# Optimization experiments

Measured on AMD Instinct MI355X. Metric: run time of the kernel, lower is better.

The kernel has to match this reference:

```python
import jax, jax.numpy as jnp
import numpy as np

N_NODES = 50000
N_EDGES = 800000
IN_DIM = 128
HID_DIM = 128
N_CLASSES = 32
X_STEPS = 2
BN_EPS = 1e-5


def _agg(h, src, dst):
    # PyG 'add' aggregation with self-loops: out[i] = sum_{(j->i) in E} h[j] + h[i]
    return jax.ops.segment_sum(h[src], dst, num_segments=h.shape[0]) + h


def setup_inputs() -> dict:
    key = jax.random.key(0)
    ks = jax.random.split(key, 8)
    x = jax.random.normal(ks[0], (N_NODES, IN_DIM), dtype=jnp.float32)
    edge_index = jax.random.randint(ks[1], (2, N_EDGES), 0, N_NODES, dtype=jnp.int64)
    s1 = 1.0 / np.sqrt(IN_DIM)
    W1 = jax.random.uniform(ks[2], (IN_DIM, HID_DIM), jnp.float32, -s1, s1)
    b1 = jax.random.uniform(ks[3], (HID_DIM,), jnp.float32, -s1, s1)
    gamma = jnp.ones((HID_DIM,), jnp.float32)
    beta = jnp.zeros((HID_DIM,), jnp.float32)
    s2 = 1.0 / np.sqrt(HID_DIM)
    W2 = jax.random.uniform(ks[4], (HID_DIM, N_CLASSES), jnp.float32, -s2, s2)
    b2 = jax.random.uniform(ks[5], (N_CLASSES,), jnp.float32, -s2, s2)
    return {"x": x, "edge_index": edge_index, "W1": W1, "b1": b1,
            "gamma": gamma, "beta": beta, "W2": W2, "b2": b2}


def reference(x, edge_index, W1, b1, gamma, beta, W2, b2):
    src, dst = edge_index[0], edge_index[1]
    # conv1: K-step sum aggregation, then Linear
    h = x
    for _ in range(X_STEPS):
        h = _agg(h, src, dst)
    h = h @ W1 + b1
    # BatchNorm (training mode: batch statistics over nodes)
    mu = jnp.mean(h, axis=0)
    var = jnp.mean(jnp.square(h - mu), axis=0)  # biased variance, as torch BN uses
    h = (h - mu) * jax.lax.rsqrt(var + BN_EPS) * gamma + beta
    h = jax.nn.selu(h)
    # dropout p=0.0 -> identity
    # conv2: 1-step aggregation + Linear
    h = _agg(h, src, dst)
    h = h @ W2 + b2
    return jax.nn.softmax(h, axis=1)
```

## Files before the change

### kernel.cpp

```cpp
#include <hip/hip_runtime.h>

#define NN 50000
#define NE 800000
#define DIM 128
#define NC 32
#define CB 782
#define CCH 13
#define EB 8192
#define NBLK 98
#define BN_EPS 1e-5f
#define SELU_ALPHA 1.6732632423543772f
#define SELU_SCALE 1.0507009873554805f

typedef __attribute__((ext_vector_type(8))) short bf16x8;
typedef __attribute__((ext_vector_type(4))) float f32x4;

#define FMA16(acc, hv, w0, w1, w2, w3)                                   \
    acc.x = fmaf(hv.x, w0.x, acc.x); acc.y = fmaf(hv.x, w0.y, acc.y);    \
    acc.z = fmaf(hv.x, w0.z, acc.z); acc.w = fmaf(hv.x, w0.w, acc.w);    \
    acc.x = fmaf(hv.y, w1.x, acc.x); acc.y = fmaf(hv.y, w1.y, acc.y);    \
    acc.z = fmaf(hv.y, w1.z, acc.z); acc.w = fmaf(hv.y, w1.w, acc.w);    \
    acc.x = fmaf(hv.z, w2.x, acc.x); acc.y = fmaf(hv.z, w2.y, acc.y);    \
    acc.z = fmaf(hv.z, w2.z, acc.z); acc.w = fmaf(hv.z, w2.w, acc.w);    \
    acc.x = fmaf(hv.w, w3.x, acc.x); acc.y = fmaf(hv.w, w3.y, acc.y);    \
    acc.z = fmaf(hv.w, w3.z, acc.z); acc.w = fmaf(hv.w, w3.w, acc.w);

#define BNSELU1(v)                                                        \
    v = v > 0.f ? SELU_SCALE * v : SELU_SCALE * SELU_ALPHA * (__expf(v) - 1.f);
#define BNSELU4(hv, sc, sh)                                               \
    hv.x = fmaf(hv.x, sc.x, sh.x); BNSELU1(hv.x)                          \
    hv.y = fmaf(hv.y, sc.y, sh.y); BNSELU1(hv.y)                          \
    hv.z = fmaf(hv.z, sc.z, sh.z); BNSELU1(hv.z)                          \
    hv.w = fmaf(hv.w, sc.w, sh.w); BNSELU1(hv.w)

__device__ __forceinline__ float bf_lo(unsigned u) { return __uint_as_float(u << 16); }
__device__ __forceinline__ float bf_hi(unsigned u) { return __uint_as_float(u & 0xffff0000u); }
__device__ __forceinline__ unsigned bf_round(float a) {
    unsigned ba = __float_as_uint(a);
    return (ba + 0x7fffu + ((ba >> 16) & 1u)) >> 16;
}
__device__ __forceinline__ unsigned pack_bf16(float a, float b) {
    return bf_round(a) | (bf_round(b) << 16);
}

__global__ void k_detect(const int* __restrict__ raw, int* __restrict__ flag,
                         float* __restrict__ z) {
    if (blockIdx.x == 0) {
        if (threadIdx.x < 64) {
            int v = raw[2 * threadIdx.x + 1];
            unsigned long long b = __ballot(v == 0);
            if (threadIdx.x == 0) *flag = (b == 0xFFFFFFFFFFFFFFFFULL) ? 1 : 0;
        }
    } else {
        z[threadIdx.x] = 0.f;
    }
}

#define CVT_BLOCKS 6250
__global__ void k_prep(const float4* __restrict__ in, uint2* __restrict__ out,
                       const float* __restrict__ W1, ushort* __restrict__ w1t) {
    if (blockIdx.x < CVT_BLOCKS) {
        int i = blockIdx.x * 256 + threadIdx.x;
        float4 v = in[i];
        out[i] = make_uint2(pack_bf16(v.x, v.y), pack_bf16(v.z, v.w));
    } else {
        int i = (blockIdx.x - CVT_BLOCKS) * 256 + threadIdx.x;
        if (i < DIM * DIM) {
            int k = i >> 7, n = i & 127;
            w1t[n * 136 + k] = (ushort)bf_round(W1[i]);
        }
    }
}

__global__ __launch_bounds__(256) void k_bcount(const void* __restrict__ raw,
                                                const int* __restrict__ flag,
                                                int* __restrict__ cnt) {
    __shared__ int lh[CB];
    int blk = blockIdx.x, tid = threadIdx.x;
    for (int t = tid; t < CB; t += 256) lh[t] = 0;
    __syncthreads();
    int f = *flag;
    const long long* r64 = (const long long*)raw;
    const int* r32 = (const int*)raw;
    int e0 = blk * EB;
    int n = min(EB, NE - e0);
    for (int i = tid; i < n; i += 256) {
        int d = f ? (int)r64[NE + e0 + i] : r32[NE + e0 + i];
        atomicAdd(&lh[d >> 6], 1);
    }
    __syncthreads();
    for (int t = tid; t < CB; t += 256) cnt[t * NBLK + blk] = lh[t];
}

__global__ void k_colscan(int* __restrict__ cnt, int* __restrict__ tot) {
    int b = blockIdx.x;
    int* row = cnt + b * NBLK;
    int l = threadIdx.x;
    int p0 = 2 * l, p1 = 2 * l + 1;
    int a0 = (p0 < NBLK) ? row[p0] : 0;
    int a1 = (p1 < NBLK) ? row[p1] : 0;
    int s = a0 + a1, inc = s;
    #pragma unroll
    for (int off = 1; off < 64; off <<= 1) {
        int u = __shfl_up(inc, off, 64);
        if (l >= off) inc += u;
    }
    int ex = inc - s;
    if (p0 < NBLK) row[p0] = ex;
    if (p1 < NBLK) row[p1] = ex + a0;
    if (l == 63) tot[b] = inc;
}

__global__ void k_cscan(const int* __restrict__ tot, int* __restrict__ cbase,
                        int* __restrict__ rowptr) {
    int lane = threadIdx.x;
    int base = lane * CCH;
    int loc[CCH];
    int s = 0;
    #pragma unroll
    for (int i = 0; i < CCH; ++i) {
        int idx = base + i;
        int v = (idx < CB) ? tot[idx] : 0;
        loc[i] = s; s += v;
    }
    int inc = s;
    #pragma unroll
    for (int off = 1; off < 64; off <<= 1) {
        int u = __shfl_up(inc, off, 64);
        if (lane >= off) inc += u;
    }
    int ex = inc - s;
    #pragma unroll
    for (int i = 0; i < CCH; ++i) {
        int idx = base + i;
        if (idx < CB) cbase[idx] = ex + loc[i];
    }
    if (lane == 63) { cbase[CB] = inc; rowptr[NN] = NE; }
}

__global__ __launch_bounds__(256) void k_cscatter2(const void* __restrict__ raw,
                                                   const int* __restrict__ flag,
                                                   const int* __restrict__ cnt,
                                                   const int* __restrict__ cbase,
                                                   unsigned* __restrict__ pairs) {
    __shared__ int lh[CB], lbase[CB], lcur[CB], gbase[CB];
    __shared__ unsigned lp[EB];
    int blk = blockIdx.x, tid = threadIdx.x;
    for (int t = tid; t < CB; t += 256) {
        lh[t] = 0;
        gbase[t] = cbase[t] + cnt[t * NBLK + blk];
    }
    __syncthreads();
    int f = *flag;
    const long long* r64 = (const long long*)raw;
    const int* r32 = (const int*)raw;
    int e0 = blk * EB;
    int n = min(EB, NE - e0);
    for (int i = tid; i < n; i += 256) {
        int d = f ? (int)r64[NE + e0 + i] : r32[NE + e0 + i];
        atomicAdd(&lh[d >> 6], 1);
    }
    __syncthreads();
    if (tid < 64) {
        int base = tid * CCH;
        int loc[CCH];
        int s = 0;
        #pragma unroll
        for (int i = 0; i < CCH; ++i) {
            int idx = base + i;
            int v = (idx < CB) ? lh[idx] : 0;
            loc[i] = s; s += v;
        }
        int inc = s;
        #pragma unroll
        for (int off = 1; off < 64; off <<= 1) {
            int u = __shfl_up(inc, off, 64);
            if (tid >= off) inc += u;
        }
        int ex = inc - s;
        #pragma unroll
        for (int i = 0; i < CCH; ++i) {
            int idx = base + i;
            if (idx < CB) lbase[idx] = ex + loc[i];
        }
    }
    __syncthreads();
    for (int t = tid; t < CB; t += 256) lcur[t] = lbase[t];
    __syncthreads();
    for (int i = tid; i < n; i += 256) {
        int d = f ? (int)r64[NE + e0 + i] : r32[NE + e0 + i];
        int sv = f ? (int)r64[e0 + i] : r32[e0 + i];
        int b = d >> 6;
        int p = atomicAdd(&lcur[b], 1);
        lp[p] = (unsigned)sv | ((unsigned)(d & 63) << 16) | ((unsigned)b << 22);
    }
    __syncthreads();
    for (int i = tid; i < n; i += 256) {
        unsigned pr = lp[i];
        int b = pr >> 22;
        pairs[gbase[b] + (i - lbase[b])] = pr;
    }
}

__global__ __launch_bounds__(256) void k_bucket(const unsigned* __restrict__ pairs,
                                                const int* __restrict__ cbase,
                                                int* __restrict__ rowptr,
                                                int* __restrict__ eidx) {
    __shared__ int cnt[64], cur[64];
    int b = blockIdx.x;
    int tid = threadIdx.x;
    if (tid < 64) cnt[tid] = 0;
    __syncthreads();
    int lo = cbase[b], hi = cbase[b + 1];
    for (int i = lo + tid; i < hi; i += 256)
        atomicAdd(&cnt[(pairs[i] >> 16) & 63], 1);
    __syncthreads();
    if (tid < 64) {
        int v = cnt[tid];
        int inc = v;
        #pragma unroll
        for (int off = 1; off < 64; off <<= 1) {
            int u = __shfl_up(inc, off, 64);
            if (tid >= off) inc += u;
        }
        int ex = inc - v;
        cur[tid] = ex;
        int node = b * 64 + tid;
        if (node < NN) rowptr[node] = lo + ex;
    }
    __syncthreads();
    for (int i = lo + tid; i < hi; i += 256) {
        unsigned pr = pairs[i];
        int p = atomicAdd(&cur[(pr >> 16) & 63], 1);
        eidx[lo + p] = (int)(pr & 0xFFFFu);
    }
}

__global__ __launch_bounds__(256) void k_gather_bf(const unsigned* __restrict__ in,
                                                   unsigned* __restrict__ out,
                                                   const int* __restrict__ rowptr,
                                                   const int* __restrict__ eidx) {
    int node = blockIdx.x * 4 + (threadIdx.x >> 6);
    if (node >= NN) return;
    int lane = threadIdx.x & 63;
    unsigned su = in[(size_t)node * 64 + lane];
    float2 acc = {bf_lo(su), bf_hi(su)};
    int b = rowptr[node], e = rowptr[node + 1];
    int j = b;
    for (; j + 3 < e; j += 4) {
        int s0 = eidx[j], s1 = eidx[j + 1], s2 = eidx[j + 2], s3 = eidx[j + 3];
        unsigned u0 = in[(size_t)s0 * 64 + lane];
        unsigned u1 = in[(size_t)s1 * 64 + lane];
        unsigned u2 = in[(size_t)s2 * 64 + lane];
        unsigned u3 = in[(size_t)s3 * 64 + lane];
        acc.x += bf_lo(u0) + bf_lo(u1) + bf_lo(u2) + bf_lo(u3);
        acc.y += bf_hi(u0) + bf_hi(u1) + bf_hi(u2) + bf_hi(u3);
    }
    for (; j < e; ++j) {
        unsigned u0 = in[(size_t)eidx[j] * 64 + lane];
        acc.x += bf_lo(u0);
        acc.y += bf_hi(u0);
    }
    out[(size_t)node * 64 + lane] = pack_bf16(acc.x, acc.y);
}

__global__ __launch_bounds__(256) void k_gemm1(
    const unsigned* __restrict__ hBb, const ushort* __restrict__ w1t,
    const float* __restrict__ b1, float* __restrict__ h1,
    float* __restrict__ ssum, float* __restrict__ ssq) {
    __shared__ __align__(16) ushort wT[DIM * 136];
    __shared__ float redS[4 * DIM];
    __shared__ float redQ[4 * DIM];
    int tid = threadIdx.x;
    for (int i = tid; i < DIM * 136 / 8; i += 256)
        ((uint4*)wT)[i] = ((const uint4*)w1t)[i];
    for (int i = tid; i < 4 * DIM; i += 256) { redS[i] = 0.f; redQ[i] = 0.f; }
    __syncthreads();

    int wid = tid >> 6, lane = tid & 63;
    int cl = lane & 15, kg = lane >> 4;
    int tile = blockIdx.x * 4 + wid;
    if (tile < NN / 16) {
        int rbase = tile * 16;
        const uint4* arow = (const uint4*)(hBb + (size_t)(rbase + cl) * 64);
        f32x4 acc[8];
        #pragma unroll
        for (int ct = 0; ct < 8; ++ct) acc[ct] = (f32x4){0.f, 0.f, 0.f, 0.f};
        #pragma unroll
        for (int kk = 0; kk < 4; ++kk) {
            union { uint4 u; bf16x8 f; } a;
            a.u = arow[kk * 4 + kg];
            #pragma unroll
            for (int ct = 0; ct < 8; ++ct) {
                union { uint4 u; bf16x8 f; } bb;
                bb.u = *(const uint4*)&wT[(ct * 16 + cl) * 136 + kk * 32 + kg * 8];
                acc[ct] = __builtin_amdgcn_mfma_f32_16x16x32_bf16(a.f, bb.f, acc[ct], 0, 0, 0);
            }
        }
        #pragma unroll
        for (int ct = 0; ct < 8; ++ct) {
            int col = ct * 16 + cl;
            float bias = b1[col];
            float s = 0.f, q = 0.f;
            #pragma unroll
            for (int i = 0; i < 4; ++i) {
                float v = acc[ct][i] + bias;
                h1[(size_t)(rbase + kg * 4 + i) * DIM + col] = v;
                s += v; q += v * v;
            }
            s += __shfl_xor(s, 16); s += __shfl_xor(s, 32);
            q += __shfl_xor(q, 16); q += __shfl_xor(q, 32);
            if (kg == 0) { redS[wid * DIM + col] = s; redQ[wid * DIM + col] = q; }
        }
    }
    __syncthreads();
    if (tid < DIM) {
        float S = redS[tid] + redS[DIM + tid] + redS[2 * DIM + tid] + redS[3 * DIM + tid];
        float Q = redQ[tid] + redQ[DIM + tid] + redQ[2 * DIM + tid] + redQ[3 * DIM + tid];
        atomicAdd(&ssum[tid], S);
        atomicAdd(&ssq[tid], Q);
    }
}

__global__ __launch_bounds__(256) void k_gemm2(const float* __restrict__ h,
                                               const float* __restrict__ W2,
                                               const float* __restrict__ ssum,
                                               const float* __restrict__ ssq,
                                               const float* __restrict__ gamma,
                                               const float* __restrict__ beta,
                                               unsigned* __restrict__ tb) {
    __shared__ float w[DIM * NC];
    __shared__ float scl[DIM], shl[DIM];
    for (int i = threadIdx.x * 4; i < DIM * NC; i += 1024)
        *(float4*)&w[i] = *(const float4*)&W2[i];
    if (threadIdx.x < DIM) {
        int c = threadIdx.x;
        float mu = ssum[c] / (float)NN;
        float var = ssq[c] / (float)NN - mu * mu;
        float rs = rsqrtf(var + BN_EPS);
        float sc = rs * gamma[c];
        scl[c] = sc;
        shl[c] = beta[c] - mu * sc;
    }
    __syncthreads();

    int c0 = (threadIdx.x & 7) * 4;
    int rg = threadIdx.x >> 3;
    int r0 = blockIdx.x * 128 + rg * 4;
    if (r0 >= NN) return;
    const float* h0 = h + (size_t)r0 * DIM;
    float4 a0 = {0, 0, 0, 0}, a1 = {0, 0, 0, 0}, a2 = {0, 0, 0, 0}, a3 = {0, 0, 0, 0};
    #pragma unroll 4
    for (int k4 = 0; k4 < DIM / 4; ++k4) {
        float4 sc = *(const float4*)&scl[k4 * 4];
        float4 sh = *(const float4*)&shl[k4 * 4];
        float4 hv0 = *(const float4*)&h0[k4 * 4];
        float4 hv1 = *(const float4*)&h0[DIM + k4 * 4];
        float4 hv2 = *(const float4*)&h0[2 * DIM + k4 * 4];
        float4 hv3 = *(const float4*)&h0[3 * DIM + k4 * 4];
        BNSELU4(hv0, sc, sh)
        BNSELU4(hv1, sc, sh)
        BNSELU4(hv2, sc, sh)
        BNSELU4(hv3, sc, sh)
        float4 w0 = *(const float4*)&w[(k4 * 4 + 0) * NC + c0];
        float4 w1 = *(const float4*)&w[(k4 * 4 + 1) * NC + c0];
        float4 w2 = *(const float4*)&w[(k4 * 4 + 2) * NC + c0];
        float4 w3 = *(const float4*)&w[(k4 * 4 + 3) * NC + c0];
        FMA16(a0, hv0, w0, w1, w2, w3)
        FMA16(a1, hv1, w0, w1, w2, w3)
        FMA16(a2, hv2, w0, w1, w2, w3)
        FMA16(a3, hv3, w0, w1, w2, w3)
    }
    ((uint2*)tb)[((size_t)r0 * 16 + c0 / 2) / 2]       = make_uint2(pack_bf16(a0.x, a0.y), pack_bf16(a0.z, a0.w));
    ((uint2*)tb)[((size_t)(r0 + 1) * 16 + c0 / 2) / 2] = make_uint2(pack_bf16(a1.x, a1.y), pack_bf16(a1.z, a1.w));
    ((uint2*)tb)[((size_t)(r0 + 2) * 16 + c0 / 2) / 2] = make_uint2(pack_bf16(a2.x, a2.y), pack_bf16(a2.z, a2.w));
    ((uint2*)tb)[((size_t)(r0 + 3) * 16 + c0 / 2) / 2] = make_uint2(pack_bf16(a3.x, a3.y), pack_bf16(a3.z, a3.w));
}

__global__ __launch_bounds__(256) void k_gsoftmax(const unsigned* __restrict__ tb,
                                                  const float* __restrict__ b2,
                                                  const int* __restrict__ rowptr,
                                                  const int* __restrict__ eidx,
                                                  float* __restrict__ out) {
    int node = blockIdx.x * 4 + (threadIdx.x >> 6);
    if (node >= NN) return;
    int lane = threadIdx.x & 63;
    int c2 = lane & 15;
    int g = lane >> 4;
    float2 acc = {0.f, 0.f};
    if (g == 0) {
        unsigned u = tb[(size_t)node * 16 + c2];
        acc.x = bf_lo(u); acc.y = bf_hi(u);
    }
    int b = rowptr[node], e = rowptr[node + 1];
    for (int j = b + g; j < e; j += 4) {
        unsigned u = tb[(size_t)eidx[j] * 16 + c2];
        acc.x += bf_lo(u);
        acc.y += bf_hi(u);
    }
    acc.x += __shfl_xor(acc.x, 16); acc.x += __shfl_xor(acc.x, 32);
    acc.y += __shfl_xor(acc.y, 16); acc.y += __shfl_xor(acc.y, 32);
    acc.x += b2[2 * c2];
    acc.y += b2[2 * c2 + 1];
    float m = fmaxf(acc.x, acc.y);
    #pragma unroll
    for (int off = 8; off; off >>= 1) m = fmaxf(m, __shfl_xor(m, off, 16));
    float2 ex = {__expf(acc.x - m), __expf(acc.y - m)};
    float s = ex.x + ex.y;
    #pragma unroll
    for (int off = 8; off; off >>= 1) s += __shfl_xor(s, off, 16);
    float inv = 1.f / s;
    if (g == 0)
        *(float2*)&out[(size_t)node * NC + 2 * c2] = make_float2(ex.x * inv, ex.y * inv);
}

extern "C" void kernel_launch(void* const* d_in, const int* in_sizes, int n_in,
                              void* d_out, int out_size, void* d_ws, size_t ws_size,
                              hipStream_t stream) {
    const float* x     = (const float*)d_in[0];
    const void*  eraw  = d_in[1];
    const float* W1    = (const float*)d_in[2];
    const float* b1    = (const float*)d_in[3];
    const float* gamma = (const float*)d_in[4];
    const float* beta  = (const float*)d_in[5];
    const float* W2    = (const float*)d_in[6];
    const float* b2    = (const float*)d_in[7];
    float* out = (float*)d_out;

    float*    regA = (float*)d_ws;
    unsigned* xb   = (unsigned*)regA;
    unsigned* hAb  = xb + (size_t)NN * 64;
    float*    h1   = regA;
    float*    regB = regA + (size_t)NN * DIM;
    unsigned* pairs= (unsigned*)regB;
    unsigned* hBb  = (unsigned*)regB;
    unsigned* tb   = (unsigned*)(regB + (size_t)NN * 64);
    int* eidx   = (int*)(regB + (size_t)NN * DIM);
    int* rowptr = eidx + NE;
    int* cnt    = rowptr + NN + 4;
    int* tot    = cnt + CB * NBLK;
    int* cbase  = tot + 784;
    float* ssum  = (float*)(cbase + 784);
    float* ssq   = ssum + DIM;
    ushort* w1t  = (ushort*)(ssq + DIM);
    int*   flag  = (int*)((char*)w1t + DIM * 136 * sizeof(ushort));

    k_detect<<<2, 256, 0, stream>>>((const int*)eraw, flag, ssum);
    k_bcount<<<NBLK, 256, 0, stream>>>(eraw, flag, cnt);
    k_colscan<<<CB, 64, 0, stream>>>(cnt, tot);
    k_cscan<<<1, 64, 0, stream>>>(tot, cbase, rowptr);
    k_cscatter2<<<NBLK, 256, 0, stream>>>(eraw, flag, cnt, cbase, pairs);
    k_bucket<<<CB, 256, 0, stream>>>(pairs, cbase, rowptr, eidx);

    k_prep<<<CVT_BLOCKS + 64, 256, 0, stream>>>((const float4*)x, (uint2*)xb, W1, w1t);

    const int gather_blocks = (NN + 3) / 4;
    k_gather_bf<<<gather_blocks, 256, 0, stream>>>(xb, hAb, rowptr, eidx);
    k_gather_bf<<<gather_blocks, 256, 0, stream>>>(hAb, hBb, rowptr, eidx);
    k_gemm1<<<(NN / 16 + 3) / 4, 256, 0, stream>>>(hBb, w1t, b1, h1, ssum, ssq);
    k_gemm2<<<(NN + 127) / 128, 256, 0, stream>>>(h1, W2, ssum, ssq, gamma, beta, tb);
    k_gsoftmax<<<gather_blocks, 256, 0, stream>>>(tb, b2, rowptr, eidx, out);
}
```

Baseline: 218.9 us.

## Fuse detect/count into prep, shrink edge indices to 16-bit, unroll gathers

Merges the dtype-detect, zero-init and bucket-count kernels into the prep kernel, and recomputes the edge-dtype flag inline with a wave ballot instead of a separate kernel and a global flag. The destination-sorted source index array goes from int to ushort, halving index traffic in the three gather kernels. The gather loop gains an 8-way unroll and the softmax gather a 2-way unroll to keep more loads in flight. 16-bit indices only hold node ids below 65536 (50000 here), and storing them as ushort moves the rowptr offset, so buffer alignment changes.

```diff
diff --git a/kernel.cpp b/kernel.cpp
--- a/kernel.cpp
+++ b/kernel.cpp
@@ -43,53 +43,46 @@
     return bf_round(a) | (bf_round(b) << 16);
 }
 
-__global__ void k_detect(const int* __restrict__ raw, int* __restrict__ flag,
-                         float* __restrict__ z) {
-    if (blockIdx.x == 0) {
-        if (threadIdx.x < 64) {
-            int v = raw[2 * threadIdx.x + 1];
-            unsigned long long b = __ballot(v == 0);
-            if (threadIdx.x == 0) *flag = (b == 0xFFFFFFFFFFFFFFFFULL) ? 1 : 0;
-        }
-    } else {
-        z[threadIdx.x] = 0.f;
-    }
+__device__ __forceinline__ int edge_flag(const int* raw) {
+    int v = raw[2 * (threadIdx.x & 63) + 1];
+    unsigned long long b = __ballot(v == 0);
+    return b == 0xFFFFFFFFFFFFFFFFULL;
 }
 
 #define CVT_BLOCKS 6250
-__global__ void k_prep(const float4* __restrict__ in, uint2* __restrict__ out,
-                       const float* __restrict__ W1, ushort* __restrict__ w1t) {
-    if (blockIdx.x < CVT_BLOCKS) {
-        int i = blockIdx.x * 256 + threadIdx.x;
+#define PREP_BLOCKS (CVT_BLOCKS + 65)
+__global__ __launch_bounds__(256) void k_prep(
+    const float4* __restrict__ in, uint2* __restrict__ out,
+    const float* __restrict__ W1, ushort* __restrict__ w1t,
+    float* __restrict__ z, const void* __restrict__ raw, int* __restrict__ cnt) {
+    __shared__ int lh[CB];
+    int bid = blockIdx.x, tid = threadIdx.x;
+    if (bid < CVT_BLOCKS) {
+        int i = bid * 256 + tid;
         float4 v = in[i];
         out[i] = make_uint2(pack_bf16(v.x, v.y), pack_bf16(v.z, v.w));
+    } else if (bid < CVT_BLOCKS + 64) {
+        int i = (bid - CVT_BLOCKS) * 256 + tid;
+        int k = i >> 7, n = i & 127;
+        w1t[n * 136 + k] = (ushort)bf_round(W1[i]);
+    } else if (bid == CVT_BLOCKS + 64) {
+        z[tid] = 0.f;
     } else {
-        int i = (blockIdx.x - CVT_BLOCKS) * 256 + threadIdx.x;
-        if (i < DIM * DIM) {
-            int k = i >> 7, n = i & 127;
-            w1t[n * 136 + k] = (ushort)bf_round(W1[i]);
-        }
-    }
-}
-
-__global__ __launch_bounds__(256) void k_bcount(const void* __restrict__ raw,
-                                                const int* __restrict__ flag,
-                                                int* __restrict__ cnt) {
-    __shared__ int lh[CB];
-    int blk = blockIdx.x, tid = threadIdx.x;
-    for (int t = tid; t < CB; t += 256) lh[t] = 0;
-    __syncthreads();
-    int f = *flag;
-    const long long* r64 = (const long long*)raw;
-    const int* r32 = (const int*)raw;
-    int e0 = blk * EB;
-    int n = min(EB, NE - e0);
-    for (int i = tid; i < n; i += 256) {
-        int d = f ? (int)r64[NE + e0 + i] : r32[NE + e0 + i];
-        atomicAdd(&lh[d >> 6], 1);
-    }
-    __syncthreads();
-    for (int t = tid; t < CB; t += 256) cnt[t * NBLK + blk] = lh[t];
+        int blk = bid - PREP_BLOCKS;
+        for (int t = tid; t < CB; t += 256) lh[t] = 0;
+        __syncthreads();
+        int f = edge_flag((const int*)raw);
+        const long long* r64 = (const long long*)raw;
+        const int* r32 = (const int*)raw;
+        int e0 = blk * EB;
+        int n = min(EB, NE - e0);
+        for (int i = tid; i < n; i += 256) {
+            int d = f ? (int)r64[NE + e0 + i] : r32[NE + e0 + i];
+            atomicAdd(&lh[d >> 6], 1);
+        }
+        __syncthreads();
+        for (int t = tid; t < CB; t += 256) cnt[t * NBLK + blk] = lh[t];
+    }
 }
 
 __global__ void k_colscan(int* __restrict__ cnt, int* __restrict__ tot) {
@@ -139,7 +132,6 @@
 }
 
 __global__ __launch_bounds__(256) void k_cscatter2(const void* __restrict__ raw,
-                                                   const int* __restrict__ flag,
                                                    const int* __restrict__ cnt,
                                                    const int* __restrict__ cbase,
                                                    unsigned* __restrict__ pairs) {
@@ -151,7 +143,7 @@
         gbase[t] = cbase[t] + cnt[t * NBLK + blk];
     }
     __syncthreads();
-    int f = *flag;
+    int f = edge_flag((const int*)raw);
     const long long* r64 = (const long long*)raw;
     const int* r32 = (const int*)raw;
     int e0 = blk * EB;
@@ -205,7 +197,7 @@
 __global__ __launch_bounds__(256) void k_bucket(const unsigned* __restrict__ pairs,
                                                 const int* __restrict__ cbase,
                                                 int* __restrict__ rowptr,
-                                                int* __restrict__ eidx) {
+                                                ushort* __restrict__ eidx) {
     __shared__ int cnt[64], cur[64];
     int b = blockIdx.x;
     int tid = threadIdx.x;
@@ -232,14 +224,14 @@
     for (int i = lo + tid; i < hi; i += 256) {
         unsigned pr = pairs[i];
         int p = atomicAdd(&cur[(pr >> 16) & 63], 1);
-        eidx[lo + p] = (int)(pr & 0xFFFFu);
+        eidx[lo + p] = (ushort)(pr & 0xFFFFu);
     }
 }
 
 __global__ __launch_bounds__(256) void k_gather_bf(const unsigned* __restrict__ in,
                                                    unsigned* __restrict__ out,
                                                    const int* __restrict__ rowptr,
-                                                   const int* __restrict__ eidx) {
+                                                   const ushort* __restrict__ eidx) {
     int node = blockIdx.x * 4 + (threadIdx.x >> 6);
     if (node >= NN) return;
     int lane = threadIdx.x & 63;
@@ -247,6 +239,22 @@
     float2 acc = {bf_lo(su), bf_hi(su)};
     int b = rowptr[node], e = rowptr[node + 1];
     int j = b;
+    for (; j + 7 < e; j += 8) {
+        int s0 = eidx[j],     s1 = eidx[j + 1], s2 = eidx[j + 2], s3 = eidx[j + 3];
+        int s4 = eidx[j + 4], s5 = eidx[j + 5], s6 = eidx[j + 6], s7 = eidx[j + 7];
+        unsigned u0 = in[(size_t)s0 * 64 + lane];
+        unsigned u1 = in[(size_t)s1 * 64 + lane];
+        unsigned u2 = in[(size_t)s2 * 64 + lane];
+        unsigned u3 = in[(size_t)s3 * 64 + lane];
+        unsigned u4 = in[(size_t)s4 * 64 + lane];
+        unsigned u5 = in[(size_t)s5 * 64 + lane];
+        unsigned u6 = in[(size_t)s6 * 64 + lane];
+        unsigned u7 = in[(size_t)s7 * 64 + lane];
+        acc.x += bf_lo(u0) + bf_lo(u1) + bf_lo(u2) + bf_lo(u3)
+               + bf_lo(u4) + bf_lo(u5) + bf_lo(u6) + bf_lo(u7);
+        acc.y += bf_hi(u0) + bf_hi(u1) + bf_hi(u2) + bf_hi(u3)
+               + bf_hi(u4) + bf_hi(u5) + bf_hi(u6) + bf_hi(u7);
+    }
     for (; j + 3 < e; j += 4) {
         int s0 = eidx[j], s1 = eidx[j + 1], s2 = eidx[j + 2], s3 = eidx[j + 3];
         unsigned u0 = in[(size_t)s0 * 64 + lane];
@@ -380,7 +388,7 @@
 __global__ __launch_bounds__(256) void k_gsoftmax(const unsigned* __restrict__ tb,
                                                   const float* __restrict__ b2,
                                                   const int* __restrict__ rowptr,
-                                                  const int* __restrict__ eidx,
+                                                  const ushort* __restrict__ eidx,
                                                   float* __restrict__ out) {
     int node = blockIdx.x * 4 + (threadIdx.x >> 6);
     if (node >= NN) return;
@@ -393,7 +401,16 @@
         acc.x = bf_lo(u); acc.y = bf_hi(u);
     }
     int b = rowptr[node], e = rowptr[node + 1];
-    for (int j = b + g; j < e; j += 4) {
+    int j = b + g;
+    for (; j + 4 < e; j += 8) {
+        int s0 = eidx[j];
+        int s1 = eidx[j + 4];
+        unsigned u0 = tb[(size_t)s0 * 16 + c2];
+        unsigned u1 = tb[(size_t)s1 * 16 + c2];
+        acc.x += bf_lo(u0) + bf_lo(u1);
+        acc.y += bf_hi(u0) + bf_hi(u1);
+    }
+    if (j < e) {
         unsigned u = tb[(size_t)eidx[j] * 16 + c2];
         acc.x += bf_lo(u);
         acc.y += bf_hi(u);
@@ -435,24 +452,21 @@
     unsigned* pairs= (unsigned*)regB;
     unsigned* hBb  = (unsigned*)regB;
     unsigned* tb   = (unsigned*)(regB + (size_t)NN * 64);
-    int* eidx   = (int*)(regB + (size_t)NN * DIM);
-    int* rowptr = eidx + NE;
+    ushort* eidx = (ushort*)(regB + (size_t)NN * DIM);
+    int* rowptr = (int*)(eidx + NE);
     int* cnt    = rowptr + NN + 4;
     int* tot    = cnt + CB * NBLK;
     int* cbase  = tot + 784;
     float* ssum  = (float*)(cbase + 784);
     float* ssq   = ssum + DIM;
     ushort* w1t  = (ushort*)(ssq + DIM);
-    int*   flag  = (int*)((char*)w1t + DIM * 136 * sizeof(ushort));
-
-    k_detect<<<2, 256, 0, stream>>>((const int*)eraw, flag, ssum);
-    k_bcount<<<NBLK, 256, 0, stream>>>(eraw, flag, cnt);
+
+    k_prep<<<PREP_BLOCKS + NBLK, 256, 0, stream>>>(
+        (const float4*)x, (uint2*)xb, W1, w1t, ssum, eraw, cnt);
     k_colscan<<<CB, 64, 0, stream>>>(cnt, tot);
     k_cscan<<<1, 64, 0, stream>>>(tot, cbase, rowptr);
-    k_cscatter2<<<NBLK, 256, 0, stream>>>(eraw, flag, cnt, cbase, pairs);
+    k_cscatter2<<<NBLK, 256, 0, stream>>>(eraw, cnt, cbase, pairs);
     k_bucket<<<CB, 256, 0, stream>>>(pairs, cbase, rowptr, eidx);
-
-    k_prep<<<CVT_BLOCKS + 64, 256, 0, stream>>>((const float4*)x, (uint2*)xb, W1, w1t);
 
     const int gather_blocks = (NN + 3) / 4;
     k_gather_bf<<<gather_blocks, 256, 0, stream>>>(xb, hAb, rowptr, eidx);
```

After: 202.3 us (median of 2 runs). -7.6%, faster.
